# Kernel tuning notes

Hardware: AMD Instinct MI355X
Metric: run time of the kernel (lower is better)

## Reference

```python
import jax, jax.numpy as jnp
import numpy as np
import math

B, S, D, H = 2, 2048, 1024, 32
HD = D // H  # head_dim = 32
NEG = -1e9


def setup_inputs() -> dict:
    key = jax.random.key(0)
    ks = jax.random.split(key, 6)
    x = jax.random.normal(ks[0], (B, S, D), dtype=jnp.float32)
    # additive causal mask: 0 on/below diagonal, -1e9 above
    causal = jnp.tril(jnp.ones((S, S), dtype=bool))
    mask = jnp.where(causal, 0.0, NEG).astype(jnp.float32)[None, None]
    # SSMax-style per-query-position log-length scale
    section_log_len = jnp.log(jnp.arange(1, S + 1, dtype=jnp.float32) + 1.0).reshape(1, 1, S, 1)
    sc = 1.0 / math.sqrt(D)
    wq = jax.random.normal(ks[1], (D, D), dtype=jnp.float32) * sc
    wk = jax.random.normal(ks[2], (D, D), dtype=jnp.float32) * sc
    wv = jax.random.normal(ks[3], (D, D), dtype=jnp.float32) * sc
    wo = jax.random.normal(ks[4], (D, D), dtype=jnp.float32) * sc
    seq_scale = jnp.ones((1, H, 1, 1), dtype=jnp.float32)
    return {"x": x, "mask": mask, "section_log_len": section_log_len,
            "wq": wq, "wk": wk, "wv": wv, "wo": wo, "seq_scale": seq_scale}


def reference(x, mask, section_log_len, wq, wk, wv, wo, seq_scale):
    bsz, seqlen, dim = x.shape
    # projections (torch Linear: y = x @ W.T); split heads -> [b, h, s, hd]
    q = (x @ wq.T).reshape(bsz, seqlen, H, HD).transpose(0, 2, 1, 3)
    k = (x @ wk.T).reshape(bsz, seqlen, H, HD).transpose(0, 2, 1, 3)
    v = (x @ wv.T).reshape(bsz, seqlen, H, HD).transpose(0, 2, 1, 3)
    # n_kv_heads == n_heads, so repeat_kv is identity
    scores = jnp.einsum('bhqd,bhkd->bhqk', q, k) / math.sqrt(HD)
    scores = scores * (section_log_len * seq_scale)  # SSMax per-head learned scale
    scores = scores + mask
    probs = jax.nn.softmax(scores.astype(jnp.float32), axis=-1).astype(q.dtype)
    out = jnp.einsum('bhqk,bhkd->bhqd', probs, v)
    out = out.transpose(0, 2, 1, 3).reshape(bsz, seqlen, dim)
    return out @ wo.T
```

## Files before the change

### kernel.cpp

```cpp
#include <hip/hip_runtime.h>
#include <hip/hip_bf16.h>

typedef __bf16 bf16_t;
typedef bf16_t bf16x8 __attribute__((ext_vector_type(8)));
typedef float f32x4 __attribute__((ext_vector_type(4)));

#define NB 2
#define SEQ 2048
#define DIM 1024
#define NH 32
#define HDIM 32

#define LDA 40

static __device__ __forceinline__ f32x4 mfma16(bf16x8 a, bf16x8 b, f32x4 c) {
    return __builtin_amdgcn_mfma_f32_16x16x32_bf16(a, b, c, 0, 0, 0);
}

static __device__ __forceinline__ void load_lds16(const bf16_t* g, bf16_t* l) {
    __builtin_amdgcn_global_load_lds(
        (const __attribute__((address_space(1))) void*)(g),
        (__attribute__((address_space(3))) void*)(l), 16, 0, 0);
}

__global__ __launch_bounds__(256)
void cvt_f32_bf16(const float* __restrict__ s0, bf16_t* __restrict__ d0, int n0,
                  const float* __restrict__ s1, bf16_t* __restrict__ d1, int n1,
                  const float* __restrict__ s2, bf16_t* __restrict__ d2, int n2,
                  const float* __restrict__ s3, bf16_t* __restrict__ d3, int n3,
                  const float* __restrict__ s4, bf16_t* __restrict__ d4, int n4) {
    const int stride = gridDim.x * blockDim.x;
    const int tid = blockIdx.x * blockDim.x + threadIdx.x;
    const float* src[5] = {s0, s1, s2, s3, s4};
    bf16_t* dst[5] = {d0, d1, d2, d3, d4};
    const int n[5] = {n0, n1, n2, n3, n4};
#pragma unroll
    for (int r = 0; r < 5; r++) {
        const int nv = n[r] >> 2;
        for (int i = tid; i < nv; i += stride) {
            float4 v = ((const float4*)src[r])[i];
            bf16_t o[4] = {(bf16_t)v.x, (bf16_t)v.y, (bf16_t)v.z, (bf16_t)v.w};
            *(uint2*)(dst[r] + i * 4) = *(const uint2*)o;
        }
    }
}

template <int EPI>
__global__ __launch_bounds__(256)
void gemm128(const bf16_t* __restrict__ A, const bf16_t* __restrict__ W,
             float* __restrict__ Cf, bf16_t* __restrict__ qb,
             bf16_t* __restrict__ kb, bf16_t* __restrict__ vtb) {
    __shared__ alignas(16) bf16_t As[128 * 32];
    __shared__ alignas(16) bf16_t Bs[128 * 32];
    const int t = threadIdx.x;
    const int lane = t & 63, wave = t >> 6;
    const int lane16 = lane & 15, quad = lane >> 4;
    const int wm = (wave >> 1) * 64, wn = (wave & 1) * 64;
    const int m0 = blockIdx.y * 128;
    const int n0g = blockIdx.x * 128;
    const int tr = t >> 2;
    const int tc = (t & 3) * 8;
    bf16_t* ldsA = As + (t & 192) * 8;
    bf16_t* ldsB = Bs + (t & 192) * 8;
    const bf16_t* ga = A + (m0 + tr) * DIM + tc;
    const bf16_t* gb = W + (n0g + tr) * DIM + tc;

    const bool vseg = (EPI == 1) && (n0g >= 2048);

    f32x4 acc[4][4];
#pragma unroll
    for (int i = 0; i < 4; i++)
#pragma unroll
        for (int j = 0; j < 4; j++) acc[i][j] = f32x4{0.f, 0.f, 0.f, 0.f};

    for (int k0 = 0; k0 < DIM; k0 += 32) {
        __syncthreads();
        load_lds16(ga + k0, ldsA);
        load_lds16(ga + 64 * DIM + k0, ldsA + 64 * 32);
        load_lds16(gb + k0, ldsB);
        load_lds16(gb + 64 * DIM + k0, ldsB + 64 * 32);
        __syncthreads();
        bf16x8 af[4], bfr[4];
#pragma unroll
        for (int mi = 0; mi < 4; mi++)
            af[mi] = *(const bf16x8*)(As + (wm + mi * 16 + lane16) * 32 + quad * 8);
#pragma unroll
        for (int ni = 0; ni < 4; ni++)
            bfr[ni] = *(const bf16x8*)(Bs + (wn + ni * 16 + lane16) * 32 + quad * 8);
        if (vseg) {
#pragma unroll
            for (int mi = 0; mi < 4; mi++)
#pragma unroll
                for (int ni = 0; ni < 4; ni++)
                    acc[mi][ni] = mfma16(bfr[ni], af[mi], acc[mi][ni]);
        } else {
#pragma unroll
            for (int mi = 0; mi < 4; mi++)
#pragma unroll
                for (int ni = 0; ni < 4; ni++)
                    acc[mi][ni] = mfma16(af[mi], bfr[ni], acc[mi][ni]);
        }
    }

    if (EPI == 0) {
#pragma unroll
        for (int mi = 0; mi < 4; mi++)
#pragma unroll
            for (int ni = 0; ni < 4; ni++)
#pragma unroll
                for (int r = 0; r < 4; r++) {
                    int row = m0 + wm + mi * 16 + quad * 4 + r;
                    int col = n0g + wn + ni * 16 + lane16;
                    Cf[row * DIM + col] = acc[mi][ni][r];
                }
    } else if (!vseg) {
        bf16_t* dst = (n0g < 1024) ? qb : kb;
        const int nb = n0g & 1023;
#pragma unroll
        for (int mi = 0; mi < 4; mi++)
#pragma unroll
            for (int ni = 0; ni < 4; ni++)
#pragma unroll
                for (int r = 0; r < 4; r++) {
                    int m = m0 + wm + mi * 16 + quad * 4 + r;
                    int nl = nb + wn + ni * 16 + lane16;
                    int b = m >> 11, s = m & (SEQ - 1);
                    int h = nl >> 5, d = nl & 31;
                    dst[(((b * NH + h) << 11) + s) * 32 + d] = (bf16_t)acc[mi][ni][r];
                }
    } else {
        const int nb = n0g & 1023;
#pragma unroll
        for (int mi = 0; mi < 4; mi++)
#pragma unroll
            for (int ni = 0; ni < 4; ni++)
#pragma unroll
                for (int r = 0; r < 4; r++) {
                    int nl = nb + wn + ni * 16 + quad * 4 + r;
                    int m = m0 + wm + mi * 16 + lane16;
                    int b = m >> 11, s = m & (SEQ - 1);
                    int h = nl >> 5, d = nl & 31;
                    vtb[(((b * NH + h) << 5) + d) * SEQ + s] = (bf16_t)acc[mi][ni][r];
                }
    }
}

__global__ __launch_bounds__(256)
void attn_fwd(const bf16_t* __restrict__ q, const bf16_t* __restrict__ k,
              const bf16_t* __restrict__ vt, const float* __restrict__ slen,
              const float* __restrict__ sscale, bf16_t* __restrict__ out) {
    __shared__ alignas(16) bf16_t pscr[4][32 * LDA];
    const int t = threadIdx.x;
    const int lane = t & 63, wave = t >> 6;
    const int lane16 = lane & 15, quad = lane >> 4;
    const int gw = blockIdx.x * 4 + wave;
    const int idx = gw & 63;
    const int qt = (idx & 1) ? (63 - (idx >> 1)) : (idx >> 1);
    const int h = (gw >> 6) & (NH - 1);
    const int b = gw >> 11;
    const int q0 = qt * 32;
    const bf16_t* qh = q + (b * NH + h) * SEQ * HDIM;
    const bf16_t* kh = k + (b * NH + h) * SEQ * HDIM;
    const bf16_t* vth = vt + (b * NH + h) * HDIM * SEQ;
    bf16_t* psw = pscr[wave];

    bf16x8 qf[2];
    qf[0] = *(const bf16x8*)(qh + (q0 + lane16) * HDIM + quad * 8);
    qf[1] = *(const bf16x8*)(qh + (q0 + 16 + lane16) * HDIM + quad * 8);

    const float hs = sscale[h] * 0.17677669529663687f * 1.4426950408889634f;
    float rs[2][4];
#pragma unroll
    for (int mi = 0; mi < 2; mi++)
#pragma unroll
        for (int r = 0; r < 4; r++)
            rs[mi][r] = slen[q0 + mi * 16 + quad * 4 + r] * hs;

    f32x4 o[2][2];
    float lrow[2][4];
#pragma unroll
    for (int mi = 0; mi < 2; mi++)
#pragma unroll
        for (int r = 0; r < 4; r++) lrow[mi][r] = 0.f;
#pragma unroll
    for (int mi = 0; mi < 2; mi++)
#pragma unroll
        for (int ni = 0; ni < 2; ni++) o[mi][ni] = f32x4{0.f, 0.f, 0.f, 0.f};

    const bf16_t* kp0 = kh + (2 * lane16) * HDIM + quad * 8;
    const bf16_t* vp0 = vth + lane16 * SEQ + quad * 8;
    const bf16_t* vp1 = vth + (16 + lane16) * SEQ + quad * 8;

    auto process = [&](bf16x8 kf0, bf16x8 kf1, int kv, bool domask) {
        const f32x4 zz = f32x4{0.f, 0.f, 0.f, 0.f};
        f32x4 sc[2][2];
        sc[0][0] = mfma16(qf[0], kf0, zz);
        sc[0][1] = mfma16(qf[0], kf1, zz);
        sc[1][0] = mfma16(qf[1], kf0, zz);
        sc[1][1] = mfma16(qf[1], kf1, zz);
        bf16x8 vf0 = *(const bf16x8*)(vp0 + kv);
        bf16x8 vf1 = *(const bf16x8*)(vp1 + kv);
#pragma unroll
        for (int mi = 0; mi < 2; mi++)
#pragma unroll
            for (int r = 0; r < 4; r++) {
                float p0 = exp2f(sc[mi][0][r] * rs[mi][r]);
                float p1 = exp2f(sc[mi][1][r] * rs[mi][r]);
                if (domask) {
                    const int rowloc = mi * 16 + quad * 4 + r;
                    if (2 * lane16 > rowloc) p0 = 0.f;
                    if (2 * lane16 + 1 > rowloc) p1 = 0.f;
                }
                lrow[mi][r] += p0 + p1;
                bf16_t pb[2] = {(bf16_t)p0, (bf16_t)p1};
                *(unsigned int*)(psw + (mi * 16 + quad * 4 + r) * LDA +
                                 2 * lane16) = *(const unsigned int*)pb;
            }
        asm volatile("s_waitcnt lgkmcnt(0)" ::: "memory");
        bf16x8 pf0 = *(const bf16x8*)(psw + lane16 * LDA + quad * 8);
        bf16x8 pf1 = *(const bf16x8*)(psw + (16 + lane16) * LDA + quad * 8);
        o[0][0] = mfma16(pf0, vf0, o[0][0]);
        o[0][1] = mfma16(pf0, vf1, o[0][1]);
        o[1][0] = mfma16(pf1, vf0, o[1][0]);
        o[1][1] = mfma16(pf1, vf1, o[1][1]);
    };

    bf16x8 kc0 = *(const bf16x8*)(kp0);
    bf16x8 kc1 = *(const bf16x8*)(kp0 + HDIM);
    for (int kv = 0; kv < q0; kv += 32) {
        bf16x8 kn0 = *(const bf16x8*)(kp0 + (kv + 32) * HDIM);
        bf16x8 kn1 = *(const bf16x8*)(kp0 + (kv + 32) * HDIM + HDIM);
        process(kc0, kc1, kv, false);
        kc0 = kn0;
        kc1 = kn1;
    }
    process(kc0, kc1, q0, true);

#pragma unroll
    for (int mi = 0; mi < 2; mi++)
#pragma unroll
        for (int r = 0; r < 4; r++) {
            float l = lrow[mi][r];
#pragma unroll
            for (int off = 1; off < 16; off <<= 1) l += __shfl_xor(l, off);
            float inv = 1.0f / l;
            int qi = q0 + mi * 16 + quad * 4 + r;
            bf16_t* ob = out + (b * SEQ + qi) * DIM + h * HDIM;
#pragma unroll
            for (int ni = 0; ni < 2; ni++)
                ob[ni * 16 + lane16] = (bf16_t)(o[mi][ni][r] * inv);
        }
}

extern "C" void kernel_launch(void* const* d_in, const int* in_sizes, int n_in,
                              void* d_out, int out_size, void* d_ws, size_t ws_size,
                              hipStream_t stream) {
    const float* x = (const float*)d_in[0];
    const float* slen = (const float*)d_in[2];
    const float* wq = (const float*)d_in[3];
    const float* wk = (const float*)d_in[4];
    const float* wv = (const float*)d_in[5];
    const float* wo = (const float*)d_in[6];
    const float* ss = (const float*)d_in[7];

    const size_t ELEMS = (size_t)NB * SEQ * DIM;
    const size_t WELEMS = (size_t)DIM * DIM;
    bf16_t* xb = (bf16_t*)d_ws;
    bf16_t* abuf = xb;
    bf16_t* wqkvb = xb + ELEMS;
    bf16_t* wob = wqkvb + 3 * WELEMS;
    bf16_t* qbuf = wob + WELEMS;
    bf16_t* vtbuf = qbuf + ELEMS;
    bf16_t* kbuf = (bf16_t*)d_out;

    dim3 blk(256);
    cvt_f32_bf16<<<dim3(1024), blk, 0, stream>>>(
        x, xb, (int)ELEMS, wq, wqkvb, (int)WELEMS, wk, wqkvb + WELEMS,
        (int)WELEMS, wv, wqkvb + 2 * WELEMS, (int)WELEMS, wo, wob, (int)WELEMS);

    gemm128<1><<<dim3(3 * DIM / 128, (NB * SEQ) / 128), blk, 0, stream>>>(
        xb, wqkvb, nullptr, qbuf, kbuf, vtbuf);
    attn_fwd<<<dim3(NB * NH * (SEQ / 32) / 4), blk, 0, stream>>>(
        qbuf, kbuf, vtbuf, slen, ss, abuf);
    gemm128<0><<<dim3(DIM / 128, (NB * SEQ) / 128), blk, 0, stream>>>(
        abuf, wob, (float*)d_out, nullptr, nullptr, nullptr);
}
```

Baseline: 235.0 us.

## Double GEMM K-step to 64, add XCD-aware block mapping, use __expf in attention

The GEMM kernel now stages 64 K-elements per iteration, which halves the number of barrier pairs and doubles the MFMA work between syncs. Blocks are remapped from a 2D grid to a 1D id, with the id's low three bits picking the M tile. This is meant to make blocks on the same XCD share weight columns and improve L2 reuse. The attention softmax swaps exp2f with a folded log2e factor for __expf with the factor dropped, which is mathematically equivalent but may change the instruction sequence. The costs are doubled LDS use per block, which may lower occupancy, and a mapping that hard-codes the M tile count of 32.

```diff
diff --git a/kernel.cpp b/kernel.cpp
--- a/kernel.cpp
+++ b/kernel.cpp
@@ -47,24 +47,25 @@
 
 template <int EPI>
 __global__ __launch_bounds__(256)
-void gemm128(const bf16_t* __restrict__ A, const bf16_t* __restrict__ W,
-             float* __restrict__ Cf, bf16_t* __restrict__ qb,
-             bf16_t* __restrict__ kb, bf16_t* __restrict__ vtb) {
-    __shared__ alignas(16) bf16_t As[128 * 32];
-    __shared__ alignas(16) bf16_t Bs[128 * 32];
+void gemm_k64(const bf16_t* __restrict__ A, const bf16_t* __restrict__ W,
+              float* __restrict__ Cf, bf16_t* __restrict__ qb,
+              bf16_t* __restrict__ kb, bf16_t* __restrict__ vtb) {
+    __shared__ alignas(16) bf16_t As[2 * 128 * 32];
+    __shared__ alignas(16) bf16_t Bs[2 * 128 * 32];
     const int t = threadIdx.x;
-    const int lane = t & 63, wave = t >> 6;
+    const int lane = t & 63;
     const int lane16 = lane & 15, quad = lane >> 4;
-    const int wm = (wave >> 1) * 64, wn = (wave & 1) * 64;
-    const int m0 = blockIdx.y * 128;
-    const int n0g = blockIdx.x * 128;
+    const int wm = ((t >> 6) >> 1) * 64, wn = ((t >> 6) & 1) * 64;
+    const int id = blockIdx.x;
+    const int xcd = id & 7, slot = id >> 3;
+    const int m0 = (xcd + 8 * (slot & 3)) * 128;
+    const int n0g = (slot >> 2) * 128;
     const int tr = t >> 2;
     const int tc = (t & 3) * 8;
     bf16_t* ldsA = As + (t & 192) * 8;
     bf16_t* ldsB = Bs + (t & 192) * 8;
     const bf16_t* ga = A + (m0 + tr) * DIM + tc;
     const bf16_t* gb = W + (n0g + tr) * DIM + tc;
-
     const bool vseg = (EPI == 1) && (n0g >= 2048);
 
     f32x4 acc[4][4];
@@ -73,32 +74,41 @@
 #pragma unroll
         for (int j = 0; j < 4; j++) acc[i][j] = f32x4{0.f, 0.f, 0.f, 0.f};
 
-    for (int k0 = 0; k0 < DIM; k0 += 32) {
+    for (int k0 = 0; k0 < DIM; k0 += 64) {
         __syncthreads();
         load_lds16(ga + k0, ldsA);
-        load_lds16(ga + 64 * DIM + k0, ldsA + 64 * 32);
+        load_lds16(ga + 64 * DIM + k0, ldsA + 2048);
+        load_lds16(ga + k0 + 32, ldsA + 4096);
+        load_lds16(ga + 64 * DIM + k0 + 32, ldsA + 6144);
         load_lds16(gb + k0, ldsB);
-        load_lds16(gb + 64 * DIM + k0, ldsB + 64 * 32);
+        load_lds16(gb + 64 * DIM + k0, ldsB + 2048);
+        load_lds16(gb + k0 + 32, ldsB + 4096);
+        load_lds16(gb + 64 * DIM + k0 + 32, ldsB + 6144);
         __syncthreads();
-        bf16x8 af[4], bfr[4];
-#pragma unroll
-        for (int mi = 0; mi < 4; mi++)
-            af[mi] = *(const bf16x8*)(As + (wm + mi * 16 + lane16) * 32 + quad * 8);
-#pragma unroll
-        for (int ni = 0; ni < 4; ni++)
-            bfr[ni] = *(const bf16x8*)(Bs + (wn + ni * 16 + lane16) * 32 + quad * 8);
-        if (vseg) {
+#pragma unroll
+        for (int p = 0; p < 2; p++) {
+            bf16x8 af[4], bfr[4];
 #pragma unroll
             for (int mi = 0; mi < 4; mi++)
-#pragma unroll
-                for (int ni = 0; ni < 4; ni++)
-                    acc[mi][ni] = mfma16(bfr[ni], af[mi], acc[mi][ni]);
-        } else {
-#pragma unroll
-            for (int mi = 0; mi < 4; mi++)
-#pragma unroll
-                for (int ni = 0; ni < 4; ni++)
-                    acc[mi][ni] = mfma16(af[mi], bfr[ni], acc[mi][ni]);
+                af[mi] = *(const bf16x8*)(As + p * 4096 +
+                                          (wm + mi * 16 + lane16) * 32 + quad * 8);
+#pragma unroll
+            for (int ni = 0; ni < 4; ni++)
+                bfr[ni] = *(const bf16x8*)(Bs + p * 4096 +
+                                           (wn + ni * 16 + lane16) * 32 + quad * 8);
+            if (vseg) {
+#pragma unroll
+                for (int mi = 0; mi < 4; mi++)
+#pragma unroll
+                    for (int ni = 0; ni < 4; ni++)
+                        acc[mi][ni] = mfma16(bfr[ni], af[mi], acc[mi][ni]);
+            } else {
+#pragma unroll
+                for (int mi = 0; mi < 4; mi++)
+#pragma unroll
+                    for (int ni = 0; ni < 4; ni++)
+                        acc[mi][ni] = mfma16(af[mi], bfr[ni], acc[mi][ni]);
+            }
         }
     }
 
@@ -168,7 +178,7 @@
     qf[0] = *(const bf16x8*)(qh + (q0 + lane16) * HDIM + quad * 8);
     qf[1] = *(const bf16x8*)(qh + (q0 + 16 + lane16) * HDIM + quad * 8);
 
-    const float hs = sscale[h] * 0.17677669529663687f * 1.4426950408889634f;
+    const float hs = sscale[h] * 0.17677669529663687f;
     float rs[2][4];
 #pragma unroll
     for (int mi = 0; mi < 2; mi++)
@@ -204,8 +214,8 @@
         for (int mi = 0; mi < 2; mi++)
 #pragma unroll
             for (int r = 0; r < 4; r++) {
-                float p0 = exp2f(sc[mi][0][r] * rs[mi][r]);
-                float p1 = exp2f(sc[mi][1][r] * rs[mi][r]);
+                float p0 = __expf(sc[mi][0][r] * rs[mi][r]);
+                float p1 = __expf(sc[mi][1][r] * rs[mi][r]);
                 if (domask) {
                     const int rowloc = mi * 16 + quad * 4 + r;
                     if (2 * lane16 > rowloc) p0 = 0.f;
@@ -278,10 +288,10 @@
         x, xb, (int)ELEMS, wq, wqkvb, (int)WELEMS, wk, wqkvb + WELEMS,
         (int)WELEMS, wv, wqkvb + 2 * WELEMS, (int)WELEMS, wo, wob, (int)WELEMS);
 
-    gemm128<1><<<dim3(3 * DIM / 128, (NB * SEQ) / 128), blk, 0, stream>>>(
-        xb, wqkvb, nullptr, qbuf, kbuf, vtbuf);
+    gemm_k64<1><<<dim3(768), blk, 0, stream>>>(xb, wqkvb, nullptr, qbuf, kbuf,
+                                               vtbuf);
     attn_fwd<<<dim3(NB * NH * (SEQ / 32) / 4), blk, 0, stream>>>(
         qbuf, kbuf, vtbuf, slen, ss, abuf);
-    gemm128<0><<<dim3(DIM / 128, (NB * SEQ) / 128), blk, 0, stream>>>(
-        abuf, wob, (float*)d_out, nullptr, nullptr, nullptr);
-}
+    gemm_k64<0><<<dim3(256), blk, 0, stream>>>(abuf, wob, (float*)d_out,
+                                               nullptr, nullptr, nullptr);
+}
```

New measurement: 221.3 us. 1.06x faster.

## Double-buffer GEMM LDS loads, XCD-aware tile mapping, fold SSMax scale into Q

Applied to the files above, without the earlier changes.

Rewrites the projection GEMM as a two-stage LDS double-buffered pipeline with explicit vmcnt waits, so global loads for the next k-slice overlap the current MFMA work. Blocks are remapped so tiles sharing A rows land on the same XCD, and the output projection uses 64-row tiles to launch more blocks. The per-position SSMax scale times 1/sqrt(hd) is folded into Q in the GEMM epilogue, which lets the attention kernel call __expf directly instead of doing a multiply and exp2. Folding the scale into bf16 Q before the dot product changes rounding slightly, and the hand-written waitcnt values must match the number of issued loads.

```diff
diff --git a/kernel.cpp b/kernel.cpp
--- a/kernel.cpp
+++ b/kernel.cpp
@@ -45,66 +45,99 @@
     }
 }
 
-template <int EPI>
+template <int EPI, int BM>
 __global__ __launch_bounds__(256)
-void gemm128(const bf16_t* __restrict__ A, const bf16_t* __restrict__ W,
-             float* __restrict__ Cf, bf16_t* __restrict__ qb,
-             bf16_t* __restrict__ kb, bf16_t* __restrict__ vtb) {
-    __shared__ alignas(16) bf16_t As[128 * 32];
-    __shared__ alignas(16) bf16_t Bs[128 * 32];
+void gemm_pipe(const bf16_t* __restrict__ A, const bf16_t* __restrict__ W,
+               float* __restrict__ Cf, bf16_t* __restrict__ qb,
+               bf16_t* __restrict__ kb, bf16_t* __restrict__ vtb,
+               const float* __restrict__ slen, const float* __restrict__ ss) {
+    constexpr int MI = BM / 32;
+    __shared__ alignas(16) bf16_t As[2 * BM * 32];
+    __shared__ alignas(16) bf16_t Bs[2 * 128 * 32];
     const int t = threadIdx.x;
     const int lane = t & 63, wave = t >> 6;
     const int lane16 = lane & 15, quad = lane >> 4;
-    const int wm = (wave >> 1) * 64, wn = (wave & 1) * 64;
-    const int m0 = blockIdx.y * 128;
-    const int n0g = blockIdx.x * 128;
+    const int wm = (wave >> 1) * (BM / 2), wn = (wave & 1) * 64;
+    const int id = blockIdx.x;
+    int m0, n0g;
+    if (EPI == 1) {
+        const int xcd = id & 7, slot = id >> 3;
+        m0 = (xcd + 8 * (slot & 3)) * 128;
+        n0g = (slot >> 2) * 128;
+    } else {
+        const int xcd = id & 7, slot = id >> 3;
+        m0 = (xcd + 8 * (slot & 7)) * 64;
+        n0g = (slot >> 3) * 128;
+    }
     const int tr = t >> 2;
     const int tc = (t & 3) * 8;
-    bf16_t* ldsA = As + (t & 192) * 8;
-    bf16_t* ldsB = Bs + (t & 192) * 8;
     const bf16_t* ga = A + (m0 + tr) * DIM + tc;
     const bf16_t* gb = W + (n0g + tr) * DIM + tc;
-
     const bool vseg = (EPI == 1) && (n0g >= 2048);
 
-    f32x4 acc[4][4];
-#pragma unroll
-    for (int i = 0; i < 4; i++)
+    f32x4 acc[MI][4];
+#pragma unroll
+    for (int i = 0; i < MI; i++)
 #pragma unroll
         for (int j = 0; j < 4; j++) acc[i][j] = f32x4{0.f, 0.f, 0.f, 0.f};
 
-    for (int k0 = 0; k0 < DIM; k0 += 32) {
-        __syncthreads();
-        load_lds16(ga + k0, ldsA);
-        load_lds16(ga + 64 * DIM + k0, ldsA + 64 * 32);
-        load_lds16(gb + k0, ldsB);
-        load_lds16(gb + 64 * DIM + k0, ldsB + 64 * 32);
-        __syncthreads();
-        bf16x8 af[4], bfr[4];
-#pragma unroll
-        for (int mi = 0; mi < 4; mi++)
-            af[mi] = *(const bf16x8*)(As + (wm + mi * 16 + lane16) * 32 + quad * 8);
+    auto stage = [&](int k0, int buf) {
+        bf16_t* a_dst = As + buf * (BM * 32) + (t & 192) * 8;
+        bf16_t* b_dst = Bs + buf * 4096 + (t & 192) * 8;
+        load_lds16(ga + k0, a_dst);
+        if (BM == 128) load_lds16(ga + 64 * DIM + k0, a_dst + 2048);
+        load_lds16(gb + k0, b_dst);
+        load_lds16(gb + 64 * DIM + k0, b_dst + 2048);
+    };
+    auto compute = [&](int buf) {
+        bf16x8 af[MI], bfr[4];
+#pragma unroll
+        for (int mi = 0; mi < MI; mi++)
+            af[mi] = *(const bf16x8*)(As + buf * (BM * 32) +
+                                      (wm + mi * 16 + lane16) * 32 + quad * 8);
 #pragma unroll
         for (int ni = 0; ni < 4; ni++)
-            bfr[ni] = *(const bf16x8*)(Bs + (wn + ni * 16 + lane16) * 32 + quad * 8);
+            bfr[ni] = *(const bf16x8*)(Bs + buf * 4096 +
+                                       (wn + ni * 16 + lane16) * 32 + quad * 8);
         if (vseg) {
 #pragma unroll
-            for (int mi = 0; mi < 4; mi++)
+            for (int mi = 0; mi < MI; mi++)
 #pragma unroll
                 for (int ni = 0; ni < 4; ni++)
                     acc[mi][ni] = mfma16(bfr[ni], af[mi], acc[mi][ni]);
         } else {
 #pragma unroll
-            for (int mi = 0; mi < 4; mi++)
+            for (int mi = 0; mi < MI; mi++)
 #pragma unroll
                 for (int ni = 0; ni < 4; ni++)
                     acc[mi][ni] = mfma16(af[mi], bfr[ni], acc[mi][ni]);
         }
+    };
+
+    stage(0, 0);
+#pragma unroll
+    for (int k0 = 0; k0 < DIM; k0 += 32) {
+        const int cur = (k0 >> 5) & 1;
+        if (k0 + 32 < DIM) {
+            stage(k0 + 32, cur ^ 1);
+            if (BM == 128)
+                asm volatile("s_waitcnt vmcnt(4)" ::: "memory");
+            else
+                asm volatile("s_waitcnt vmcnt(3)" ::: "memory");
+        } else {
+            asm volatile("s_waitcnt vmcnt(0)" ::: "memory");
+        }
+        asm volatile("s_barrier" ::: "memory");
+        compute(cur);
+        if (k0 + 32 < DIM) {
+            asm volatile("s_waitcnt lgkmcnt(0)" ::: "memory");
+            asm volatile("s_barrier" ::: "memory");
+        }
     }
 
     if (EPI == 0) {
 #pragma unroll
-        for (int mi = 0; mi < 4; mi++)
+        for (int mi = 0; mi < MI; mi++)
 #pragma unroll
             for (int ni = 0; ni < 4; ni++)
 #pragma unroll
@@ -114,24 +147,31 @@
                     Cf[row * DIM + col] = acc[mi][ni][r];
                 }
     } else if (!vseg) {
-        bf16_t* dst = (n0g < 1024) ? qb : kb;
+        const bool isq = (n0g < 1024);
+        bf16_t* dst = isq ? qb : kb;
         const int nb = n0g & 1023;
 #pragma unroll
-        for (int mi = 0; mi < 4; mi++)
-#pragma unroll
-            for (int ni = 0; ni < 4; ni++)
+        for (int mi = 0; mi < MI; mi++)
+#pragma unroll
+            for (int ni = 0; ni < 4; ni++) {
+                const int h = ((nb + wn) >> 5) + (ni >> 1);
+                const float hscale =
+                    isq ? ss[h] * 0.17677669529663687f : 0.f;
 #pragma unroll
                 for (int r = 0; r < 4; r++) {
                     int m = m0 + wm + mi * 16 + quad * 4 + r;
                     int nl = nb + wn + ni * 16 + lane16;
                     int b = m >> 11, s = m & (SEQ - 1);
-                    int h = nl >> 5, d = nl & 31;
-                    dst[(((b * NH + h) << 11) + s) * 32 + d] = (bf16_t)acc[mi][ni][r];
+                    int d = nl & 31;
+                    float v = acc[mi][ni][r];
+                    if (isq) v *= slen[s] * hscale;
+                    dst[(((b * NH + h) << 11) + s) * 32 + d] = (bf16_t)v;
                 }
+            }
     } else {
         const int nb = n0g & 1023;
 #pragma unroll
-        for (int mi = 0; mi < 4; mi++)
+        for (int mi = 0; mi < MI; mi++)
 #pragma unroll
             for (int ni = 0; ni < 4; ni++)
 #pragma unroll
@@ -147,8 +187,7 @@
 
 __global__ __launch_bounds__(256)
 void attn_fwd(const bf16_t* __restrict__ q, const bf16_t* __restrict__ k,
-              const bf16_t* __restrict__ vt, const float* __restrict__ slen,
-              const float* __restrict__ sscale, bf16_t* __restrict__ out) {
+              const bf16_t* __restrict__ vt, bf16_t* __restrict__ out) {
     __shared__ alignas(16) bf16_t pscr[4][32 * LDA];
     const int t = threadIdx.x;
     const int lane = t & 63, wave = t >> 6;
@@ -168,14 +207,6 @@
     qf[0] = *(const bf16x8*)(qh + (q0 + lane16) * HDIM + quad * 8);
     qf[1] = *(const bf16x8*)(qh + (q0 + 16 + lane16) * HDIM + quad * 8);
 
-    const float hs = sscale[h] * 0.17677669529663687f * 1.4426950408889634f;
-    float rs[2][4];
-#pragma unroll
-    for (int mi = 0; mi < 2; mi++)
-#pragma unroll
-        for (int r = 0; r < 4; r++)
-            rs[mi][r] = slen[q0 + mi * 16 + quad * 4 + r] * hs;
-
     f32x4 o[2][2];
     float lrow[2][4];
 #pragma unroll
@@ -204,8 +235,8 @@
         for (int mi = 0; mi < 2; mi++)
 #pragma unroll
             for (int r = 0; r < 4; r++) {
-                float p0 = exp2f(sc[mi][0][r] * rs[mi][r]);
-                float p1 = exp2f(sc[mi][1][r] * rs[mi][r]);
+                float p0 = __expf(sc[mi][0][r]);
+                float p1 = __expf(sc[mi][1][r]);
                 if (domask) {
                     const int rowloc = mi * 16 + quad * 4 + r;
                     if (2 * lane16 > rowloc) p0 = 0.f;
@@ -278,10 +309,10 @@
         x, xb, (int)ELEMS, wq, wqkvb, (int)WELEMS, wk, wqkvb + WELEMS,
         (int)WELEMS, wv, wqkvb + 2 * WELEMS, (int)WELEMS, wo, wob, (int)WELEMS);
 
-    gemm128<1><<<dim3(3 * DIM / 128, (NB * SEQ) / 128), blk, 0, stream>>>(
-        xb, wqkvb, nullptr, qbuf, kbuf, vtbuf);
+    gemm_pipe<1, 128><<<dim3(768), blk, 0, stream>>>(
+        xb, wqkvb, nullptr, qbuf, kbuf, vtbuf, slen, ss);
     attn_fwd<<<dim3(NB * NH * (SEQ / 32) / 4), blk, 0, stream>>>(
-        qbuf, kbuf, vtbuf, slen, ss, abuf);
-    gemm128<0><<<dim3(DIM / 128, (NB * SEQ) / 128), blk, 0, stream>>>(
-        abuf, wob, (float*)d_out, nullptr, nullptr, nullptr);
-}
+        qbuf, kbuf, vtbuf, abuf);
+    gemm_pipe<0, 64><<<dim3(512), blk, 0, stream>>>(
+        abuf, wob, (float*)d_out, nullptr, nullptr, nullptr, nullptr, nullptr);
+}
```

Measured after the change: 216.0 us. 8.1% less time.
